# Performance work log

Measured on AMD Instinct MI355X. Metric: run time of the kernel, lower is better.

## Reference

```python
import jax, jax.numpy as jnp
import numpy as np

DIM = 128
CODEBOOK_SIZE = 1024
DECAY = 0.99
EPSILON = 1e-06


def setup_inputs() -> dict:
    key = jax.random.key(0)
    k1, k2, k3, k4 = jax.random.split(key, 4)
    x = jax.random.normal(k1, (64, 1024, DIM), dtype=jnp.float32)
    embed = jax.random.normal(k2, (CODEBOOK_SIZE, DIM), dtype=jnp.float32)
    # keep all codes above the dead-code threshold (2) so expire_codes_ is a no-op
    cluster_size = jax.random.uniform(k3, (CODEBOOK_SIZE,), dtype=jnp.float32) * 10.0 + 2.0
    embed_avg = jax.random.normal(k4, (CODEBOOK_SIZE, DIM), dtype=jnp.float32)
    return {"x": x, "embed": embed, "cluster_size": cluster_size, "embed_avg": embed_avg}


def reference(x, embed, cluster_size, embed_avg):
    shape = x.shape
    xf = x.reshape(-1, shape[-1])  # [N, D]

    # quantize: squared euclidean distances [N, K] then argmin
    dist = (
        jnp.sum(xf * xf, axis=1, keepdims=True)
        - 2.0 * (xf @ embed.T)
        + jnp.sum(embed * embed, axis=1)[None, :]
    )
    embed_ind_flat = jnp.argmin(dist, axis=-1)  # [N]
    embed_ind = embed_ind_flat.reshape(shape[:-1])

    # dequantize
    quantize = embed[embed_ind]  # [..., D]

    # training EMA updates (one-hot scatter accumulation)
    one_hot_sum = jax.ops.segment_sum(
        jnp.ones_like(embed_ind_flat, dtype=x.dtype), embed_ind_flat,
        num_segments=CODEBOOK_SIZE)
    embed_sum = jax.ops.segment_sum(xf, embed_ind_flat, num_segments=CODEBOOK_SIZE)  # [K, D]

    cluster_size_new = cluster_size * DECAY + one_hot_sum * (1.0 - DECAY)
    embed_avg_new = embed_avg * DECAY + embed_sum * (1.0 - DECAY)

    total = jnp.sum(cluster_size_new)
    smoothed = (cluster_size_new + EPSILON) / (total + EPSILON * CODEBOOK_SIZE) * total
    embed_new = embed_avg_new / smoothed[:, None]

    return quantize, embed_ind, cluster_size_new, embed_avg_new, embed_new
```

## Files before the change

kernel.cpp:

```cpp
#include <hip/hip_runtime.h>
#include <hip/hip_fp16.h>
#include <float.h>

#define DIMD   128
#define KCODES 1024
#define NROWS  65536
#define TAU    0.03f
#define SEG_R  16

typedef __attribute__((ext_vector_type(8)))  _Float16 half8;
typedef __attribute__((ext_vector_type(16))) float f32x16;

union U8 { uint4 u; half8 h; };

__device__ __forceinline__ unsigned packh2(float a, float b) {
    __half2 t = __floats2half2_rn(a, b);
    return *(unsigned*)&t;
}

__global__ __launch_bounds__(256) void pre_kernel(
    const float* __restrict__ embed, uint4* __restrict__ ehg,
    float* __restrict__ enorm, uint4* __restrict__ zero_region)
{
    if (blockIdx.x < 64) {
        int t = blockIdx.x * 256 + threadIdx.x;
        int chunk = t >> 9;
        int s = (t >> 6) & 7;
        int L = t & 63;
        const float* src = embed + ((size_t)(chunk * 32 + (L & 31)) * DIMD) + s * 16 + (L >> 5) * 8;
        float4 a = *(const float4*)src;
        float4 b = *(const float4*)(src + 4);
        float f[8] = {a.x, a.y, a.z, a.w, b.x, b.y, b.z, b.w};
        uint4 H;
        unsigned* hw = (unsigned*)&H;
#pragma unroll
        for (int j = 0; j < 4; ++j) hw[j] = packh2(f[2 * j], f[2 * j + 1]);
        ehg[t] = H;
    } else if (blockIdx.x < 68) {
        int k = (blockIdx.x - 64) * 256 + threadIdx.x;
        const float4* e = (const float4*)(embed + (size_t)k * DIMD);
        float s = 0.f;
#pragma unroll
        for (int c = 0; c < DIMD / 4; ++c) {
            float4 v = e[c];
            s += v.x * v.x + v.y * v.y + v.z * v.z + v.w * v.w;
        }
        enorm[k] = s;
    } else {
        uint4 z = {0, 0, 0, 0};
        zero_region[threadIdx.x] = z;
        zero_region[threadIdx.x + 256] = z;
    }
}

__global__ __launch_bounds__(256, 2) void argmin_mfma(
    const float* __restrict__ x, const uint4* __restrict__ ehg,
    const float* __restrict__ enorm,
    int* __restrict__ ind_i, float* __restrict__ ind_f,
    int* __restrict__ wl, int* __restrict__ wl_cnt)
{
    __shared__ uint4 Bs[512];

    const int tid  = threadIdx.x;
    const int wave = tid >> 6;
    const int lane = tid & 63;
    const int n    = lane & 31;
    const int h    = lane >> 5;
    const int row0 = blockIdx.x * 128;
    const int rowA = row0 + wave * 32 + n;

    uint4 xh[8], xl[8];
    const float* xrow = x + (size_t)rowA * DIMD + h * 8;
#pragma unroll
    for (int s = 0; s < 8; ++s) {
        float4 a = *(const float4*)(xrow + s * 16);
        float4 b = *(const float4*)(xrow + s * 16 + 4);
        float f[8] = {a.x, a.y, a.z, a.w, b.x, b.y, b.z, b.w};
        unsigned* ph = (unsigned*)&xh[s];
        unsigned* pl = (unsigned*)&xl[s];
#pragma unroll
        for (int j = 0; j < 4; ++j) {
            float u0 = f[2 * j], u1 = f[2 * j + 1];
            __half2 hh = __floats2half2_rn(u0, u1);
            ph[j] = *(unsigned*)&hh;
            float2 back = __half22float2(hh);
            __half2 ll = __floats2half2_rn(u0 - back.x, u1 - back.y);
            pl[j] = *(unsigned*)&ll;
        }
    }

    float bestv[16], best2[16];
    int   besti[16];
#pragma unroll
    for (int r = 0; r < 16; ++r) { bestv[r] = FLT_MAX; best2[r] = FLT_MAX; besti[r] = 0; }

    for (int chunk = 0; chunk < KCODES / 32; ++chunk) {
        __syncthreads();
        {
            const uint4* sh = ehg + chunk * 512;
            Bs[tid]       = sh[tid];
            Bs[tid + 256] = sh[tid + 256];
        }
        float ee_val = enorm[chunk * 32 + n];
        __syncthreads();

        f32x16 acc;
#pragma unroll
        for (int r = 0; r < 16; ++r) acc[r] = 0.f;

#pragma unroll
        for (int s = 0; s < 8; ++s) {
            U8 ah, al, bh;
            ah.u = xh[s]; al.u = xl[s];
            bh.u = Bs[s * 64 + lane];
            acc = __builtin_amdgcn_mfma_f32_32x32x16_f16(ah.h, bh.h, acc, 0, 0, 0);
            acc = __builtin_amdgcn_mfma_f32_32x32x16_f16(al.h, bh.h, acc, 0, 0, 0);
        }

        const int nglob = chunk * 32 + n;
#pragma unroll
        for (int r = 0; r < 16; ++r) {
            float d = fmaf(-2.f, acc[r], ee_val);
            bool c1 = d < bestv[r];
            float t = c1 ? bestv[r] : d;
            best2[r] = fminf(best2[r], t);
            besti[r] = c1 ? nglob : besti[r];
            bestv[r] = fminf(bestv[r], d);
        }
    }

#pragma unroll
    for (int m = 1; m <= 16; m <<= 1) {
#pragma unroll
        for (int r = 0; r < 16; ++r) {
            float ov = __shfl_xor(bestv[r], m, 64);
            float o2 = __shfl_xor(best2[r], m, 64);
            int   oi = __shfl_xor(besti[r], m, 64);
            float hi = fmaxf(bestv[r], ov);
            best2[r] = fminf(fminf(best2[r], o2), hi);
            bool take = (ov < bestv[r]) || (ov == bestv[r] && oi < besti[r]);
            bestv[r] = take ? ov : bestv[r];
            besti[r] = take ? oi : besti[r];
        }
    }

    if (n == 0) {
#pragma unroll
        for (int r = 0; r < 16; ++r) {
            int row = row0 + wave * 32 + (r & 3) + 8 * (r >> 2) + 4 * h;
            ind_i[row] = besti[r];
            ind_f[row] = (float)besti[r];
            if (best2[r] - bestv[r] < TAU) {
                int p = atomicAdd(wl_cnt, 1);
                if (p < NROWS) wl[p] = row;
            }
        }
    }
}

__global__ __launch_bounds__(256) void recheck_kernel(
    const float* __restrict__ x, const float* __restrict__ embed,
    const float* __restrict__ enorm, const int* __restrict__ wl,
    const int* __restrict__ wl_cnt, int* __restrict__ ind_i, float* __restrict__ ind_f)
{
    __shared__ float xs[DIMD];
    __shared__ float rv[256];
    __shared__ int   ri[256];
    const int tid = threadIdx.x;
    int count = *wl_cnt;
    if (count > NROWS) count = NROWS;

    for (int i = blockIdx.x; i < count; i += gridDim.x) {
        const int row = wl[i];
        __syncthreads();
        if (tid < DIMD) xs[tid] = x[(size_t)row * DIMD + tid];
        __syncthreads();

        const float4* xs4 = (const float4*)xs;
        float xn = 0.f;
#pragma unroll 8
        for (int c = 0; c < 32; ++c) {
            float4 v = xs4[c];
            xn += v.x * v.x + v.y * v.y + v.z * v.z + v.w * v.w;
        }

        float bv = FLT_MAX; int bi = 0;
#pragma unroll
        for (int c = 0; c < 4; ++c) {
            int code = tid * 4 + c;
            const float4* er = (const float4*)(embed + (size_t)code * DIMD);
            float acc = 0.f;
#pragma unroll 8
            for (int kk = 0; kk < 32; ++kk) {
                float4 a = xs4[kk];
                float4 b = er[kk];
                acc += a.x * b.x + a.y * b.y + a.z * b.z + a.w * b.w;
            }
            float d = (xn - 2.0f * acc) + enorm[code];
            if (d < bv) { bv = d; bi = code; }
        }
        rv[tid] = bv; ri[tid] = bi;
        __syncthreads();
        for (int s = 128; s > 0; s >>= 1) {
            if (tid < s) {
                if (rv[tid + s] < rv[tid] || (rv[tid + s] == rv[tid] && ri[tid + s] < ri[tid])) {
                    rv[tid] = rv[tid + s]; ri[tid] = ri[tid + s];
                }
            }
            __syncthreads();
        }
        if (tid == 0) {
            int s_new = ri[0];
            if (s_new != ind_i[row]) {
                ind_i[row] = s_new;
                ind_f[row] = (float)s_new;
            }
        }
        __syncthreads();
    }
}

__global__ __launch_bounds__(256) void hist_kernel(
    const int* __restrict__ ind, int* __restrict__ counts)
{
    __shared__ int hcnt[KCODES];
    for (int i = threadIdx.x; i < KCODES; i += 256) hcnt[i] = 0;
    __syncthreads();
    const int base = blockIdx.x * 2048;
    for (int i = threadIdx.x; i < 2048; i += 256) atomicAdd(&hcnt[ind[base + i]], 1);
    __syncthreads();
    for (int i = threadIdx.x; i < KCODES; i += 256) {
        int v = hcnt[i];
        if (v) atomicAdd(&counts[i], v);
    }
}

__global__ __launch_bounds__(1024) void scan_cluster_kernel(
    const int* __restrict__ counts, const float* __restrict__ cluster_size,
    int* __restrict__ cursor, float* __restrict__ out_cs, float* __restrict__ smoothed)
{
    __shared__ int   s[KCODES];
    __shared__ float rf[KCODES];
    const int t = threadIdx.x;
    int my = counts[t];
    s[t] = my;
    float cs = cluster_size[t] * 0.99f + (float)my * 0.01f;
    out_cs[t] = cs;
    rf[t] = cs;
    __syncthreads();
    for (int d = 1; d < KCODES; d <<= 1) {
        int v = (t >= d) ? s[t - d] : 0;
        __syncthreads();
        s[t] += v;
        __syncthreads();
    }
    cursor[t] = s[t] - my;
    for (int st = 512; st > 0; st >>= 1) {
        if (t < st) rf[t] += rf[t + st];
        __syncthreads();
    }
    float total = rf[0];
    smoothed[t] = (cs + 1e-6f) / (total + 1e-6f * (float)KCODES) * total;
}

__global__ __launch_bounds__(256) void permbuild_kernel(
    const int* __restrict__ ind, int* __restrict__ cursor,
    int* __restrict__ perm, int* __restrict__ codes, uint4* __restrict__ embed_sum4)
{
    const int tid = threadIdx.x;
    if (tid < 128) {
        uint4 z = {0, 0, 0, 0};
        embed_sum4[blockIdx.x * 128 + tid] = z;
    }
    const int row = blockIdx.x * 256 + tid;
    const int k = ind[row];
    int pos = atomicAdd(&cursor[k], 1);
    perm[pos] = row;
    codes[pos] = k;
}

__global__ __launch_bounds__(256) void segsum_kernel(
    const float* __restrict__ x, const float* __restrict__ embed,
    const int* __restrict__ perm, const int* __restrict__ codes,
    float* __restrict__ embed_sum, float* __restrict__ out_q)
{
    const int g = (blockIdx.x * 256 + threadIdx.x) >> 5;
    const int c = threadIdx.x & 31;
    const int base = g * SEG_R;

    float4 acc = {0.f, 0.f, 0.f, 0.f};
    int curk = codes[base];
#pragma unroll
    for (int j = 0; j < SEG_R; ++j) {
        int r = perm[base + j];
        int k = codes[base + j];
        float4 v = *(const float4*)(x + (size_t)r * DIMD + c * 4);
        float4 e = *(const float4*)(embed + (size_t)k * DIMD + c * 4);
        *(float4*)(out_q + (size_t)r * DIMD + c * 4) = e;
        if (k != curk) {
            float* dst = embed_sum + (size_t)curk * DIMD + c * 4;
            atomicAdd(dst + 0, acc.x);
            atomicAdd(dst + 1, acc.y);
            atomicAdd(dst + 2, acc.z);
            atomicAdd(dst + 3, acc.w);
            acc = v;
            curk = k;
        } else {
            acc.x += v.x; acc.y += v.y; acc.z += v.z; acc.w += v.w;
        }
    }
    float* dst = embed_sum + (size_t)curk * DIMD + c * 4;
    atomicAdd(dst + 0, acc.x);
    atomicAdd(dst + 1, acc.y);
    atomicAdd(dst + 2, acc.z);
    atomicAdd(dst + 3, acc.w);
}

__global__ void embed_kernel(
    const float* __restrict__ embed_avg, const float* __restrict__ embed_sum,
    const float* __restrict__ smoothed, float* __restrict__ out_ea,
    float* __restrict__ out_en)
{
    int i = blockIdx.x * blockDim.x + threadIdx.x;
    if (i < KCODES * DIMD) {
        float ea = embed_avg[i] * 0.99f + embed_sum[i] * 0.01f;
        out_ea[i] = ea;
        out_en[i] = ea / smoothed[i >> 7];
    }
}

extern "C" void kernel_launch(void* const* d_in, const int* in_sizes, int n_in,
                              void* d_out, int out_size, void* d_ws, size_t ws_size,
                              hipStream_t stream) {
    const float* x            = (const float*)d_in[0];
    const float* embed        = (const float*)d_in[1];
    const float* cluster_size = (const float*)d_in[2];
    const float* embed_avg    = (const float*)d_in[3];

    float* out     = (float*)d_out;
    float* out_q   = out;
    float* out_ind = out + 8388608;
    float* out_cs  = out + 8454144;
    float* out_ea  = out + 8455168;
    float* out_en  = out + 8586240;

    char* ws = (char*)d_ws;
    int*   ind_i     = (int*)(ws + 0);
    float* enorm     = (float*)(ws + 262144);
    int*   countsI   = (int*)(ws + 266240);
    int*   wl_cnt    = (int*)(ws + 270336);
    int*   cursor    = (int*)(ws + 274432);
    float* smoothed  = (float*)(ws + 278528);
    int*   perm      = (int*)(ws + 286720);
    int*   wl        = (int*)(ws + 548864);
    int*   codes     = (int*)(ws + 548864);
    uint4* ehg       = (uint4*)(ws + 811008);
    float* embed_sum = (float*)(ws + 811008);

    pre_kernel<<<69, 256, 0, stream>>>(embed, ehg, enorm, (uint4*)countsI);
    argmin_mfma<<<NROWS / 128, 256, 0, stream>>>(
        x, ehg, enorm, ind_i, out_ind, wl, wl_cnt);
    recheck_kernel<<<512, 256, 0, stream>>>(
        x, embed, enorm, wl, wl_cnt, ind_i, out_ind);
    hist_kernel<<<32, 256, 0, stream>>>(ind_i, countsI);
    scan_cluster_kernel<<<1, 1024, 0, stream>>>(countsI, cluster_size, cursor, out_cs, smoothed);
    permbuild_kernel<<<NROWS / 256, 256, 0, stream>>>(
        ind_i, cursor, perm, codes, (uint4*)embed_sum);
    segsum_kernel<<<(NROWS / SEG_R) * 32 / 256, 256, 0, stream>>>(
        x, embed, perm, codes, embed_sum, out_q);
    embed_kernel<<<(KCODES * DIMD + 255) / 256, 256, 0, stream>>>(
        embed_avg, embed_sum, smoothed, out_ea, out_en);
}
```

Before: 243.0 us.

## Fuse post-argmin stages into one persistent kernel with grid barriers

Replaces the recheck, histogram, scan/cluster, permutation-build, segment-sum and embed-update kernels with one persistent 512-block kernel. The stages are separated by a software grid barrier built on an atomic counter with acquire spin-waits. The permutation build also moves to a per-block shared-memory histogram that reserves cursor ranges with one global atomic per code, instead of one per row. This aims to remove several kernel launch gaps, at the cost of barrier spin overhead, reliance on all 512 blocks being co-resident, and more global atomics in the smaller per-block histogram.

```diff
diff --git a/kernel.cpp b/kernel.cpp
--- a/kernel.cpp
+++ b/kernel.cpp
@@ -7,6 +7,7 @@
 #define NROWS  65536
 #define TAU    0.03f
 #define SEG_R  16
+#define MEGAB  512
 
 typedef __attribute__((ext_vector_type(8)))  _Float16 half8;
 typedef __attribute__((ext_vector_type(16))) float f32x16;
@@ -158,171 +159,211 @@
     }
 }
 
-__global__ __launch_bounds__(256) void recheck_kernel(
+__device__ __forceinline__ void gsync(int* bar, int target) {
+    __syncthreads();
+    if (threadIdx.x == 0) {
+        __threadfence();
+        atomicAdd(bar, 1);
+        while (__hip_atomic_load(bar, __ATOMIC_ACQUIRE, __HIP_MEMORY_SCOPE_AGENT) < target) {
+            __builtin_amdgcn_s_sleep(2);
+        }
+    }
+    __syncthreads();
+    __threadfence();
+}
+
+__global__ __launch_bounds__(256) void mega_kernel(
     const float* __restrict__ x, const float* __restrict__ embed,
-    const float* __restrict__ enorm, const int* __restrict__ wl,
-    const int* __restrict__ wl_cnt, int* __restrict__ ind_i, float* __restrict__ ind_f)
+    const float* __restrict__ cluster_size, const float* __restrict__ embed_avg,
+    const float* __restrict__ enorm,
+    int* __restrict__ ind_i, float* __restrict__ ind_f,
+    const int* __restrict__ wl, const int* __restrict__ wl_cnt,
+    int* __restrict__ counts, int* __restrict__ cursor, float* __restrict__ smoothed,
+    int* __restrict__ perm, int* __restrict__ codes, float* __restrict__ embed_sum,
+    float* __restrict__ out_q, float* __restrict__ out_cs,
+    float* __restrict__ out_ea, float* __restrict__ out_en,
+    int* __restrict__ bar)
 {
     __shared__ float xs[DIMD];
     __shared__ float rv[256];
     __shared__ int   ri[256];
+    __shared__ int   hcnt[KCODES];
+    __shared__ int   hbase[KCODES];
+    __shared__ int   ssum[256];
+    __shared__ float tred[256];
+
     const int tid = threadIdx.x;
-    int count = *wl_cnt;
-    if (count > NROWS) count = NROWS;
-
-    for (int i = blockIdx.x; i < count; i += gridDim.x) {
-        const int row = wl[i];
-        __syncthreads();
-        if (tid < DIMD) xs[tid] = x[(size_t)row * DIMD + tid];
-        __syncthreads();
-
-        const float4* xs4 = (const float4*)xs;
-        float xn = 0.f;
+    const int bid = blockIdx.x;
+
+    {
+        int count = *wl_cnt;
+        if (count > NROWS) count = NROWS;
+        for (int i = bid; i < count; i += MEGAB) {
+            const int row = wl[i];
+            __syncthreads();
+            if (tid < DIMD) xs[tid] = x[(size_t)row * DIMD + tid];
+            __syncthreads();
+            const float4* xs4 = (const float4*)xs;
+            float xn = 0.f;
 #pragma unroll 8
-        for (int c = 0; c < 32; ++c) {
-            float4 v = xs4[c];
-            xn += v.x * v.x + v.y * v.y + v.z * v.z + v.w * v.w;
-        }
-
-        float bv = FLT_MAX; int bi = 0;
-#pragma unroll
-        for (int c = 0; c < 4; ++c) {
-            int code = tid * 4 + c;
-            const float4* er = (const float4*)(embed + (size_t)code * DIMD);
-            float acc = 0.f;
+            for (int c = 0; c < 32; ++c) {
+                float4 v = xs4[c];
+                xn += v.x * v.x + v.y * v.y + v.z * v.z + v.w * v.w;
+            }
+            float bv = FLT_MAX; int bi = 0;
+#pragma unroll
+            for (int c = 0; c < 4; ++c) {
+                int code = tid * 4 + c;
+                const float4* er = (const float4*)(embed + (size_t)code * DIMD);
+                float acc = 0.f;
 #pragma unroll 8
-            for (int kk = 0; kk < 32; ++kk) {
-                float4 a = xs4[kk];
-                float4 b = er[kk];
-                acc += a.x * b.x + a.y * b.y + a.z * b.z + a.w * b.w;
-            }
-            float d = (xn - 2.0f * acc) + enorm[code];
-            if (d < bv) { bv = d; bi = code; }
-        }
-        rv[tid] = bv; ri[tid] = bi;
+                for (int kk = 0; kk < 32; ++kk) {
+                    float4 a = xs4[kk];
+                    float4 b = er[kk];
+                    acc += a.x * b.x + a.y * b.y + a.z * b.z + a.w * b.w;
+                }
+                float d = (xn - 2.0f * acc) + enorm[code];
+                if (d < bv) { bv = d; bi = code; }
+            }
+            rv[tid] = bv; ri[tid] = bi;
+            __syncthreads();
+            for (int s = 128; s > 0; s >>= 1) {
+                if (tid < s) {
+                    if (rv[tid + s] < rv[tid] || (rv[tid + s] == rv[tid] && ri[tid + s] < ri[tid])) {
+                        rv[tid] = rv[tid + s]; ri[tid] = ri[tid + s];
+                    }
+                }
+                __syncthreads();
+            }
+            if (tid == 0) {
+                int s_new = ri[0];
+                if (s_new != ind_i[row]) {
+                    ind_i[row] = s_new;
+                    ind_f[row] = (float)s_new;
+                }
+            }
+        }
+    }
+    gsync(bar, MEGAB * 1);
+
+    {
+#pragma unroll
+        for (int i = 0; i < 4; ++i) hcnt[tid + 256 * i] = 0;
+        __syncthreads();
+        if (tid < 128) atomicAdd(&hcnt[ind_i[bid * 128 + tid]], 1);
+        __syncthreads();
+#pragma unroll
+        for (int i = 0; i < 4; ++i) {
+            int k = tid + 256 * i;
+            int v = hcnt[k];
+            if (v) atomicAdd(&counts[k], v);
+        }
+    }
+    gsync(bar, MEGAB * 2);
+
+    if (bid == 0) {
+        int c[4];
+#pragma unroll
+        for (int j = 0; j < 4; ++j) c[j] = counts[4 * tid + j];
+        int s0 = c[0], s1 = s0 + c[1], s2 = s1 + c[2], s3 = s2 + c[3];
+        ssum[tid] = s3;
+        __syncthreads();
+        for (int d = 1; d < 256; d <<= 1) {
+            int v = (tid >= d) ? ssum[tid - d] : 0;
+            __syncthreads();
+            ssum[tid] += v;
+            __syncthreads();
+        }
+        int base = ssum[tid] - s3;
+        cursor[4 * tid + 0] = base;
+        cursor[4 * tid + 1] = base + s0;
+        cursor[4 * tid + 2] = base + s1;
+        cursor[4 * tid + 3] = base + s2;
+        float cs[4], csum = 0.f;
+#pragma unroll
+        for (int j = 0; j < 4; ++j) {
+            cs[j] = cluster_size[4 * tid + j] * 0.99f + (float)c[j] * 0.01f;
+            out_cs[4 * tid + j] = cs[j];
+            csum += cs[j];
+        }
+        tred[tid] = csum;
         __syncthreads();
         for (int s = 128; s > 0; s >>= 1) {
-            if (tid < s) {
-                if (rv[tid + s] < rv[tid] || (rv[tid + s] == rv[tid] && ri[tid + s] < ri[tid])) {
-                    rv[tid] = rv[tid + s]; ri[tid] = ri[tid + s];
-                }
-            }
-            __syncthreads();
-        }
-        if (tid == 0) {
-            int s_new = ri[0];
-            if (s_new != ind_i[row]) {
-                ind_i[row] = s_new;
-                ind_f[row] = (float)s_new;
-            }
-        }
-        __syncthreads();
-    }
-}
-
-__global__ __launch_bounds__(256) void hist_kernel(
-    const int* __restrict__ ind, int* __restrict__ counts)
-{
-    __shared__ int hcnt[KCODES];
-    for (int i = threadIdx.x; i < KCODES; i += 256) hcnt[i] = 0;
-    __syncthreads();
-    const int base = blockIdx.x * 2048;
-    for (int i = threadIdx.x; i < 2048; i += 256) atomicAdd(&hcnt[ind[base + i]], 1);
-    __syncthreads();
-    for (int i = threadIdx.x; i < KCODES; i += 256) {
-        int v = hcnt[i];
-        if (v) atomicAdd(&counts[i], v);
-    }
-}
-
-__global__ __launch_bounds__(1024) void scan_cluster_kernel(
-    const int* __restrict__ counts, const float* __restrict__ cluster_size,
-    int* __restrict__ cursor, float* __restrict__ out_cs, float* __restrict__ smoothed)
-{
-    __shared__ int   s[KCODES];
-    __shared__ float rf[KCODES];
-    const int t = threadIdx.x;
-    int my = counts[t];
-    s[t] = my;
-    float cs = cluster_size[t] * 0.99f + (float)my * 0.01f;
-    out_cs[t] = cs;
-    rf[t] = cs;
-    __syncthreads();
-    for (int d = 1; d < KCODES; d <<= 1) {
-        int v = (t >= d) ? s[t - d] : 0;
-        __syncthreads();
-        s[t] += v;
-        __syncthreads();
-    }
-    cursor[t] = s[t] - my;
-    for (int st = 512; st > 0; st >>= 1) {
-        if (t < st) rf[t] += rf[t + st];
-        __syncthreads();
-    }
-    float total = rf[0];
-    smoothed[t] = (cs + 1e-6f) / (total + 1e-6f * (float)KCODES) * total;
-}
-
-__global__ __launch_bounds__(256) void permbuild_kernel(
-    const int* __restrict__ ind, int* __restrict__ cursor,
-    int* __restrict__ perm, int* __restrict__ codes, uint4* __restrict__ embed_sum4)
-{
-    const int tid = threadIdx.x;
-    if (tid < 128) {
-        uint4 z = {0, 0, 0, 0};
-        embed_sum4[blockIdx.x * 128 + tid] = z;
-    }
-    const int row = blockIdx.x * 256 + tid;
-    const int k = ind[row];
-    int pos = atomicAdd(&cursor[k], 1);
-    perm[pos] = row;
-    codes[pos] = k;
-}
-
-__global__ __launch_bounds__(256) void segsum_kernel(
-    const float* __restrict__ x, const float* __restrict__ embed,
-    const int* __restrict__ perm, const int* __restrict__ codes,
-    float* __restrict__ embed_sum, float* __restrict__ out_q)
-{
-    const int g = (blockIdx.x * 256 + threadIdx.x) >> 5;
-    const int c = threadIdx.x & 31;
-    const int base = g * SEG_R;
-
-    float4 acc = {0.f, 0.f, 0.f, 0.f};
-    int curk = codes[base];
-#pragma unroll
-    for (int j = 0; j < SEG_R; ++j) {
-        int r = perm[base + j];
-        int k = codes[base + j];
-        float4 v = *(const float4*)(x + (size_t)r * DIMD + c * 4);
-        float4 e = *(const float4*)(embed + (size_t)k * DIMD + c * 4);
-        *(float4*)(out_q + (size_t)r * DIMD + c * 4) = e;
-        if (k != curk) {
-            float* dst = embed_sum + (size_t)curk * DIMD + c * 4;
-            atomicAdd(dst + 0, acc.x);
-            atomicAdd(dst + 1, acc.y);
-            atomicAdd(dst + 2, acc.z);
-            atomicAdd(dst + 3, acc.w);
-            acc = v;
-            curk = k;
-        } else {
-            acc.x += v.x; acc.y += v.y; acc.z += v.z; acc.w += v.w;
-        }
-    }
-    float* dst = embed_sum + (size_t)curk * DIMD + c * 4;
-    atomicAdd(dst + 0, acc.x);
-    atomicAdd(dst + 1, acc.y);
-    atomicAdd(dst + 2, acc.z);
-    atomicAdd(dst + 3, acc.w);
-}
-
-__global__ void embed_kernel(
-    const float* __restrict__ embed_avg, const float* __restrict__ embed_sum,
-    const float* __restrict__ smoothed, float* __restrict__ out_ea,
-    float* __restrict__ out_en)
-{
-    int i = blockIdx.x * blockDim.x + threadIdx.x;
-    if (i < KCODES * DIMD) {
+            if (tid < s) tred[tid] += tred[tid + s];
+            __syncthreads();
+        }
+        float total = tred[0];
+#pragma unroll
+        for (int j = 0; j < 4; ++j)
+            smoothed[4 * tid + j] = (cs[j] + 1e-6f) / (total + 1e-6f * (float)KCODES) * total;
+    }
+    gsync(bar, MEGAB * 3);
+
+    {
+        if (tid < 64) {
+            uint4 z = {0, 0, 0, 0};
+            ((uint4*)embed_sum)[bid * 64 + tid] = z;
+        }
+#pragma unroll
+        for (int i = 0; i < 4; ++i) hcnt[tid + 256 * i] = 0;
+        __syncthreads();
+        int row = bid * 128 + tid;
+        int k = -1;
+        if (tid < 128) {
+            k = ind_i[row];
+            atomicAdd(&hcnt[k], 1);
+        }
+        __syncthreads();
+#pragma unroll
+        for (int i = 0; i < 4; ++i) {
+            int kk = tid + 256 * i;
+            int v = hcnt[kk];
+            hbase[kk] = v ? atomicAdd(&cursor[kk], v) : 0;
+        }
+        __syncthreads();
+        if (tid < 128) {
+            int pos = atomicAdd(&hbase[k], 1);
+            perm[pos] = row;
+            codes[pos] = k;
+        }
+    }
+    gsync(bar, MEGAB * 4);
+
+    {
+        const int g = bid * 8 + (tid >> 5);
+        const int c = tid & 31;
+        const int base = g * SEG_R;
+        float4 acc = {0.f, 0.f, 0.f, 0.f};
+        int curk = codes[base];
+#pragma unroll
+        for (int j = 0; j < SEG_R; ++j) {
+            int r = perm[base + j];
+            int k = codes[base + j];
+            float4 v = *(const float4*)(x + (size_t)r * DIMD + c * 4);
+            float4 e = *(const float4*)(embed + (size_t)k * DIMD + c * 4);
+            *(float4*)(out_q + (size_t)r * DIMD + c * 4) = e;
+            if (k != curk) {
+                float* dst = embed_sum + (size_t)curk * DIMD + c * 4;
+                atomicAdd(dst + 0, acc.x);
+                atomicAdd(dst + 1, acc.y);
+                atomicAdd(dst + 2, acc.z);
+                atomicAdd(dst + 3, acc.w);
+                acc = v;
+                curk = k;
+            } else {
+                acc.x += v.x; acc.y += v.y; acc.z += v.z; acc.w += v.w;
+            }
+        }
+        float* dst = embed_sum + (size_t)curk * DIMD + c * 4;
+        atomicAdd(dst + 0, acc.x);
+        atomicAdd(dst + 1, acc.y);
+        atomicAdd(dst + 2, acc.z);
+        atomicAdd(dst + 3, acc.w);
+    }
+    gsync(bar, MEGAB * 5);
+
+    {
+        int i = bid * 256 + tid;
         float ea = embed_avg[i] * 0.99f + embed_sum[i] * 0.01f;
         out_ea[i] = ea;
         out_en[i] = ea / smoothed[i >> 7];
@@ -349,6 +390,7 @@
     float* enorm     = (float*)(ws + 262144);
     int*   countsI   = (int*)(ws + 266240);
     int*   wl_cnt    = (int*)(ws + 270336);
+    int*   bar       = (int*)(ws + 270592);
     int*   cursor    = (int*)(ws + 274432);
     float* smoothed  = (float*)(ws + 278528);
     int*   perm      = (int*)(ws + 286720);
@@ -360,14 +402,10 @@
     pre_kernel<<<69, 256, 0, stream>>>(embed, ehg, enorm, (uint4*)countsI);
     argmin_mfma<<<NROWS / 128, 256, 0, stream>>>(
         x, ehg, enorm, ind_i, out_ind, wl, wl_cnt);
-    recheck_kernel<<<512, 256, 0, stream>>>(
-        x, embed, enorm, wl, wl_cnt, ind_i, out_ind);
-    hist_kernel<<<32, 256, 0, stream>>>(ind_i, countsI);
-    scan_cluster_kernel<<<1, 1024, 0, stream>>>(countsI, cluster_size, cursor, out_cs, smoothed);
-    permbuild_kernel<<<NROWS / 256, 256, 0, stream>>>(
-        ind_i, cursor, perm, codes, (uint4*)embed_sum);
-    segsum_kernel<<<(NROWS / SEG_R) * 32 / 256, 256, 0, stream>>>(
-        x, embed, perm, codes, embed_sum, out_q);
-    embed_kernel<<<(KCODES * DIMD + 255) / 256, 256, 0, stream>>>(
-        embed_avg, embed_sum, smoothed, out_ea, out_en);
-}
+    mega_kernel<<<MEGAB, 256, 0, stream>>>(
+        x, embed, cluster_size, embed_avg, enorm,
+        ind_i, out_ind, wl, wl_cnt,
+        countsI, cursor, smoothed,
+        perm, codes, embed_sum,
+        out_q, out_cs, out_ea, out_en, bar);
+}
```

New measurement: 646.2 us. 166% more time.
